# Performance work log

Measured on AMD Instinct MI355X. Metric: run time of the kernel, lower is better.

The kernel has to match this reference:

```python
import jax, jax.numpy as jnp
import numpy as np

B, T = 2, 2048
D_MODEL = 1024
N_LAYERS = 2
VOCAB = 256
BLOCK = 2048
LOCAL = 128
STRIDE = 256
NHEAD = D_MODEL // 64  # 16
HEAD_DIM = D_MODEL // NHEAD  # 64
LN_EPS = 1e-5


def setup_inputs() -> dict:
    key = jax.random.key(0)
    ks = jax.random.split(key, 16)
    L, d = N_LAYERS, D_MODEL

    def g(k, shape, scale=0.02):
        return (jax.random.normal(k, shape, dtype=jnp.float32) * scale)

    return {
        "x": jax.random.randint(ks[0], (B, T), 0, VOCAB),
        "embed": g(ks[1], (VOCAB, d)),
        "pos_embed": g(ks[2], (BLOCK, d)),
        # per-layer weights stacked on leading L axis; Linear as y = x @ W + b
        "Wq": g(ks[3], (L, d, d)), "bq": jnp.zeros((L, d), jnp.float32),
        "Wk": g(ks[4], (L, d, d)), "bk": jnp.zeros((L, d), jnp.float32),
        "Wv": g(ks[5], (L, d, d)), "bv": jnp.zeros((L, d), jnp.float32),
        "Wo": g(ks[6], (L, d, d)), "bo": jnp.zeros((L, d), jnp.float32),
        "g1": jnp.ones((L, d), jnp.float32), "be1": jnp.zeros((L, d), jnp.float32),
        "W1": g(ks[7], (L, d, 4 * d)), "bf1": jnp.zeros((L, 4 * d), jnp.float32),
        "W2": g(ks[8], (L, 4 * d, d)), "bf2": jnp.zeros((L, d), jnp.float32),
        "g2": jnp.ones((L, d), jnp.float32), "be2": jnp.zeros((L, d), jnp.float32),
        "gf": jnp.ones((d,), jnp.float32), "bef": jnp.zeros((d,), jnp.float32),
        "Whead": g(ks[9], (d, VOCAB)),
    }


def _ln(x, gamma, beta):
    mu = jnp.mean(x, axis=-1, keepdims=True)
    var = jnp.mean(jnp.square(x - mu), axis=-1, keepdims=True)
    return (x - mu) * jax.lax.rsqrt(var + LN_EPS) * gamma + beta


def _sparse_mask(t):
    # allowed[i, j] = True if token i may attend to token j
    i = jnp.arange(t)[:, None]
    j = jnp.arange(t)[None, :]
    causal = j <= i
    local = (i - j) <= LOCAL
    glob = (j % STRIDE) == 0
    return causal & (local | glob)


def _sparse_attn(q, k, v, allowed):
    # q, k, v: [B, T, D] -> [B, H, T, hd]
    b, t, d = q.shape
    def split(x):
        return x.reshape(b, t, NHEAD, HEAD_DIM).transpose(0, 2, 1, 3)
    q, k, v = split(q), split(k), split(v)
    scale = HEAD_DIM ** -0.5
    scores = jnp.einsum("bhqd,bhkd->bhqk", q, k) * scale
    scores = jnp.where(allowed[None, None], scores, -jnp.inf)
    attn = jax.nn.softmax(scores, axis=-1)  # every row has j=i allowed -> no NaN
    out = jnp.einsum("bhqk,bhkd->bhqd", attn, v)
    return out.transpose(0, 2, 1, 3).reshape(b, t, d)


def reference(x, embed, pos_embed, Wq, bq, Wk, bk, Wv, bv, Wo, bo,
              g1, be1, W1, bf1, W2, bf2, g2, be2, gf, bef, Whead):
    b, t = x.shape
    h = embed[x] + pos_embed[jnp.arange(t)][None]
    allowed = _sparse_mask(t)
    for l in range(N_LAYERS):
        h_n = _ln(h, g1[l], be1[l])
        q = h_n @ Wq[l] + bq[l]
        k = h_n @ Wk[l] + bk[l]
        v = h_n @ Wv[l] + bv[l]
        attn_out = _sparse_attn(q, k, v, allowed)
        h = h + (attn_out @ Wo[l] + bo[l])
        h2 = _ln(h, g2[l], be2[l])
        ffn = jax.nn.gelu(h2 @ W1[l] + bf1[l], approximate=False) @ W2[l] + bf2[l]
        h = h + ffn
    h = _ln(h, gf, bef)
    return h @ Whead
```

## Files before the change

kernel.cpp:

```cpp
#include <hip/hip_runtime.h>
#include <hip/hip_bf16.h>

#define BB 2
#define TT 2048
#define DD 1024
#define FF 4096
#define VV 256
#define HH 16
#define HD 64
#define MM (BB * TT)
#define LOCAL_W 128
#define STRIDE_G 256
#define QS 3072

typedef short s16x8 __attribute__((ext_vector_type(8)));
typedef __bf16 bf16x8 __attribute__((ext_vector_type(8)));
typedef float f32x4 __attribute__((ext_vector_type(4)));

#define WAITVM(N) asm volatile("s_waitcnt vmcnt(" #N ")" ::: "memory")
#define CFENCE asm volatile("" ::: "memory")

__device__ __forceinline__ float b2f(unsigned short u) {
  return __builtin_bit_cast(float, (unsigned int)u << 16);
}
__device__ __forceinline__ unsigned short f2b(float f) {
  __hip_bfloat16 h = __float2bfloat16(f);
  return __builtin_bit_cast(unsigned short, h);
}
__device__ __forceinline__ void gl_lds16(const unsigned short* g, unsigned short* l) {
  __builtin_amdgcn_global_load_lds(
      (const __attribute__((address_space(1))) void*)g,
      (__attribute__((address_space(3))) void*)l, 16, 0, 0);
}
__device__ __forceinline__ bf16x8 ldsr(const unsigned short* p) {
  return __builtin_bit_cast(bf16x8, *(const s16x8*)p);
}

__global__ __launch_bounds__(256) void transpose_k(const float* __restrict__ W,
                                                   unsigned short* __restrict__ WT,
                                                   int K, int N,
                                                   size_t sstride, size_t dstride) {
  __shared__ float t[32][33];
  const int z = blockIdx.z;
  W += (size_t)z * sstride;
  WT += (size_t)z * dstride;
  const int n0 = blockIdx.x * 32, k0 = blockIdx.y * 32;
  const int tx = threadIdx.x, ty = threadIdx.y;
  for (int r = ty; r < 32; r += 8) t[r][tx] = W[(size_t)(k0 + r) * N + n0 + tx];
  __syncthreads();
  for (int r = ty; r < 32; r += 8)
    WT[(size_t)(n0 + r) * K + k0 + tx] = f2b(t[tx][r]);
}

__global__ __launch_bounds__(256) void qkv_t(const float* __restrict__ Wq,
                                             const float* __restrict__ Wk,
                                             const float* __restrict__ Wv,
                                             unsigned short* __restrict__ WT) {
  __shared__ float t[32][33];
  const int z = blockIdx.z;
  const int l = z / 3, which = z % 3;
  const float* W = (which == 0 ? Wq : which == 1 ? Wk : Wv) + (size_t)l * DD * DD;
  unsigned short* D = WT + ((size_t)l * QS + which * DD) * DD;
  const int n0 = blockIdx.x * 32, k0 = blockIdx.y * 32;
  const int tx = threadIdx.x, ty = threadIdx.y;
  for (int r = ty; r < 32; r += 8) t[r][tx] = W[(size_t)(k0 + r) * DD + n0 + tx];
  __syncthreads();
  for (int r = ty; r < 32; r += 8)
    D[(size_t)(n0 + r) * DD + k0 + tx] = f2b(t[tx][r]);
}

__global__ __launch_bounds__(256) void concat_bias(const float* __restrict__ bq,
                                                   const float* __restrict__ bk,
                                                   const float* __restrict__ bv,
                                                   float* __restrict__ bcat) {
  const int i = blockIdx.x * 256 + threadIdx.x;
  const int l = i / QS, j = i - l * QS;
  float v;
  if (j < DD) v = bq[l * DD + j];
  else if (j < 2 * DD) v = bk[l * DD + j - DD];
  else v = bv[l * DD + j - 2 * DD];
  bcat[i] = v;
}

__global__ __launch_bounds__(256) void embed_ln(const int* __restrict__ x,
                                                const float* __restrict__ emb,
                                                const float* __restrict__ pos,
                                                const float* __restrict__ g,
                                                const float* __restrict__ be,
                                                float* __restrict__ h,
                                                unsigned short* __restrict__ out) {
  const int row = blockIdx.x;
  const int tid = threadIdx.x;
  const int tok = x[row];
  const int t = row & (TT - 1);
  f32x4 v = *(const f32x4*)&emb[(size_t)tok * DD + tid * 4];
  v += *(const f32x4*)&pos[(size_t)t * DD + tid * 4];
  *(f32x4*)&h[(size_t)row * DD + tid * 4] = v;
  float s = v[0] + v[1] + v[2] + v[3];
  float sq = v[0] * v[0] + v[1] * v[1] + v[2] * v[2] + v[3] * v[3];
#pragma unroll
  for (int off = 32; off; off >>= 1) {
    s += __shfl_xor(s, off);
    sq += __shfl_xor(sq, off);
  }
  __shared__ float ss[4], ssq[4];
  const int w = tid >> 6, lane = tid & 63;
  if (lane == 0) { ss[w] = s; ssq[w] = sq; }
  __syncthreads();
  s = ss[0] + ss[1] + ss[2] + ss[3];
  sq = ssq[0] + ssq[1] + ssq[2] + ssq[3];
  const float mean = s * (1.0f / DD);
  const float var = sq * (1.0f / DD) - mean * mean;
  const float rstd = rsqrtf(var + 1e-5f);
  const float4 gv = *(const float4*)&g[tid * 4];
  const float4 bv = *(const float4*)&be[tid * 4];
  ushort4 o;
  o.x = f2b((v[0] - mean) * rstd * gv.x + bv.x);
  o.y = f2b((v[1] - mean) * rstd * gv.y + bv.y);
  o.z = f2b((v[2] - mean) * rstd * gv.z + bv.z);
  o.w = f2b((v[3] - mean) * rstd * gv.w + bv.w);
  *(ushort4*)&out[(size_t)row * DD + tid * 4] = o;
}

__global__ __launch_bounds__(256) void ln_red(float* __restrict__ hio,
                                              const float* __restrict__ parts,
                                              const float* __restrict__ bias,
                                              const float* __restrict__ g,
                                              const float* __restrict__ be,
                                              unsigned short* __restrict__ out) {
  const int row = blockIdx.x;
  const int tid = threadIdx.x;
  const size_t base = (size_t)row * DD + tid * 4;
  f32x4 v = *(const f32x4*)&hio[base];
  v += *(const f32x4*)&bias[tid * 4];
  v += *(const f32x4*)&parts[base];
  v += *(const f32x4*)&parts[(size_t)MM * DD + base];
  *(f32x4*)&hio[base] = v;
  float s = v[0] + v[1] + v[2] + v[3];
  float sq = v[0] * v[0] + v[1] * v[1] + v[2] * v[2] + v[3] * v[3];
#pragma unroll
  for (int off = 32; off; off >>= 1) {
    s += __shfl_xor(s, off);
    sq += __shfl_xor(sq, off);
  }
  __shared__ float ss[4], ssq[4];
  const int w = tid >> 6, lane = tid & 63;
  if (lane == 0) { ss[w] = s; ssq[w] = sq; }
  __syncthreads();
  s = ss[0] + ss[1] + ss[2] + ss[3];
  sq = ssq[0] + ssq[1] + ssq[2] + ssq[3];
  const float mean = s * (1.0f / DD);
  const float var = sq * (1.0f / DD) - mean * mean;
  const float rstd = rsqrtf(var + 1e-5f);
  const float4 gv = *(const float4*)&g[tid * 4];
  const float4 bv = *(const float4*)&be[tid * 4];
  ushort4 o;
  o.x = f2b((v[0] - mean) * rstd * gv.x + bv.x);
  o.y = f2b((v[1] - mean) * rstd * gv.y + bv.y);
  o.z = f2b((v[2] - mean) * rstd * gv.z + bv.z);
  o.w = f2b((v[3] - mean) * rstd * gv.w + bv.w);
  *(ushort4*)&out[(size_t)row * DD + tid * 4] = o;
}

template <int EPI>
__global__ __launch_bounds__(512, 4) void gemm_dw3(const unsigned short* __restrict__ A,
                                                   const unsigned short* __restrict__ BT,
                                                   const float* __restrict__ bias,
                                                   void* __restrict__ outp,
                                                   int M, int N, int K,
                                                   int nbx, int nby, int ksplit,
                                                   int ksub) {
  __shared__ __align__(16) unsigned short lds[36864];
  const int tid = threadIdx.x;
  const int lane = tid & 63;
  const int w = tid >> 6;
  const int o = blockIdx.x;
  const int xcd = o & 7;
  const int j = o >> 3;
  const int m_per = (nby * ksplit) >> 2;
  const int n_per = nbx >> 1;
  const int m_loc = j % m_per, n_loc = j / m_per;
  const int m_idx = (xcd >> 1) * m_per + m_loc;
  const int n_idx = (xcd & 1) * n_per + n_loc;
  const int ks = m_idx / nby;
  const int mp = m_idx - ks * nby;
  const int n0 = n_idx * 128;
  const int m0 = mp * 256;
  const int kb = ks * ksub;
  const int wm = w >> 1, wn = w & 1;
  f32x4 acc[4][4] = {};

  const unsigned short* aSrc[2];
  const unsigned short* bSrc;
  int dstA[2], dstB;
#pragma unroll
  for (int i = 0; i < 2; i++) {
    const int s = tid + (i << 9);
    const int row = s >> 2, sc = s & 3;
    const int l = sc ^ ((row >> 1) & 3);
    aSrc[i] = &A[(size_t)(m0 + row) * K + kb + l * 8];
    dstA[i] = s * 8;
  }
  {
    const int row = tid >> 2, sc = tid & 3;
    const int l = sc ^ ((row >> 1) & 3);
    bSrc = &BT[(size_t)(n0 + row) * K + kb + l * 8];
    dstB = 8192 + tid * 8;
  }
  auto STAGE = [&](int u, int base) {
    const int kt = u << 5;
    gl_lds16(aSrc[0] + kt, &lds[base + dstA[0]]);
    gl_lds16(aSrc[1] + kt, &lds[base + dstA[1]]);
    gl_lds16(bSrc + kt, &lds[base + dstB]);
  };

  const int rA = lane & 15, cr = lane >> 4;
  const int rowA0 = wm * 64 + rA;
  const int rowB0 = wn * 64 + rA;
  const int aAddr0 = rowA0 * 32 + ((cr ^ ((rowA0 >> 1) & 3)) << 3);
  const int bAddr0 = 8192 + rowB0 * 32 + ((cr ^ ((rowB0 >> 1) & 3)) << 3);

  const int NS = ksub >> 5;
  int c0 = 0, c1 = 12288, c2 = 24576;
  STAGE(0, c0);
  STAGE(1, c1);

  for (int u = 0; u < NS; ++u) {
    if (u + 1 < NS) { WAITVM(3); } else { WAITVM(0); }
    __builtin_amdgcn_s_barrier();
    CFENCE;
    if (u + 2 < NS) STAGE(u + 2, c2);
    bf16x8 bfr[4], af[4];
#pragma unroll
    for (int n = 0; n < 4; n++) bfr[n] = ldsr(&lds[c0 + bAddr0 + n * 512]);
#pragma unroll
    for (int i = 0; i < 4; i++) af[i] = ldsr(&lds[c0 + aAddr0 + i * 512]);
    __builtin_amdgcn_s_setprio(1);
#pragma unroll
    for (int i = 0; i < 4; i++)
#pragma unroll
      for (int n = 0; n < 4; n++)
        acc[i][n] = __builtin_amdgcn_mfma_f32_16x16x32_bf16(af[i], bfr[n], acc[i][n], 0, 0, 0);
    __builtin_amdgcn_s_setprio(0);
    const int t = c0; c0 = c1; c1 = c2; c2 = t;
  }

  const int r0 = (lane >> 4) * 4;
  const int cc = lane & 15;
#pragma unroll
  for (int m = 0; m < 4; m++)
#pragma unroll
    for (int n = 0; n < 4; n++)
#pragma unroll
      for (int r = 0; r < 4; r++) {
        const int row = m0 + wm * 64 + m * 16 + r0 + r;
        const int col = n0 + wn * 64 + n * 16 + cc;
        const size_t idx = (size_t)row * N + col;
        if (EPI == 0) {
          ((float*)outp)[(size_t)ks * M * N + idx] = acc[m][n][r];
        } else {
          float val = acc[m][n][r] + bias[col];
          if (EPI == 3) {
            float u2 = val * (0.7978845608f + 0.0356774081f * val * val);
            u2 = fminf(u2, 10.0f);
            const float e = __expf(2.0f * u2);
            val = val * e / (e + 1.0f);
          }
          ((unsigned short*)outp)[idx] = f2b(val);
        }
      }
}

__global__ __launch_bounds__(512, 2) void gemm_p(const unsigned short* __restrict__ A,
                                                 const unsigned short* __restrict__ BT,
                                                 float* __restrict__ outp,
                                                 int M, int N, int K, int nbx, int nwg2,
                                                 int ksub) {
  constexpr int BM = 128;
  __shared__ __align__(16) unsigned short lds[4][BM * 64];
  const int tid = threadIdx.x;
  const int lane = tid & 63;
  const int w = tid >> 6;
  const int nwg = gridDim.x;
  const int orig = blockIdx.x;
  const int wg = (orig & 7) * (nwg >> 3) + (orig >> 3);
  const int ks = wg / nwg2;
  const int rem = wg - ks * nwg2;
  const int n0 = (rem % nbx) * BM;
  const int m0 = (rem / nbx) * BM;
  const int kb = ks * ksub;
  const int wm = w >> 2, wn = w & 3;
  f32x4 acc[4][2] = {};

  auto STAGE = [&](int t) {
    const int b = t & 3;
    const int kt = kb + (t << 5);
    const int s = tid;
    const int row = s >> 2, sc = s & 3;
    const int c = sc ^ ((row >> 1) & 3);
    gl_lds16(&A[(size_t)(m0 + row) * K + kt + c * 8], &lds[b][s * 8]);
    gl_lds16(&BT[(size_t)(n0 + row) * K + kt + c * 8], &lds[b][BM * 32 + s * 8]);
  };

  const int NT = ksub >> 5;
  STAGE(0); STAGE(1); STAGE(2);

  for (int t = 0; t < NT; ++t) {
    const int ahead = NT - 1 - t;
    if (ahead >= 2) WAITVM(4); else if (ahead == 1) WAITVM(2); else WAITVM(0);
    __builtin_amdgcn_s_barrier();
    CFENCE;
    if (t + 3 < NT) STAGE(t + 3);
    const int b = t & 3;
    const int rA = lane & 15, cr = lane >> 4;
    bf16x8 af[4], bfr[2];
#pragma unroll
    for (int m = 0; m < 4; m++) {
      const int row = wm * 64 + m * 16 + rA;
      af[m] = ldsr(&lds[b][row * 32 + ((cr ^ ((row >> 1) & 3)) << 3)]);
    }
#pragma unroll
    for (int n = 0; n < 2; n++) {
      const int row = wn * 32 + n * 16 + rA;
      bfr[n] = ldsr(&lds[b][BM * 32 + row * 32 + ((cr ^ ((row >> 1) & 3)) << 3)]);
    }
    __builtin_amdgcn_s_setprio(1);
#pragma unroll
    for (int m = 0; m < 4; m++)
#pragma unroll
      for (int n = 0; n < 2; n++)
        acc[m][n] = __builtin_amdgcn_mfma_f32_16x16x32_bf16(af[m], bfr[n], acc[m][n], 0, 0, 0);
    __builtin_amdgcn_s_setprio(0);
  }

  const int r0 = (lane >> 4) * 4;
  const int cc = lane & 15;
  float* pout = outp + (size_t)ks * M * N;
#pragma unroll
  for (int m = 0; m < 4; m++)
#pragma unroll
    for (int n = 0; n < 2; n++)
#pragma unroll
      for (int r = 0; r < 4; r++) {
        const int row = m0 + wm * 64 + m * 16 + r0 + r;
        const int col = n0 + wn * 32 + n * 16 + cc;
        pout[(size_t)row * N + col] = acc[m][n][r];
      }
}

template <int NP>
__global__ __launch_bounds__(256) void reduce_k(float* __restrict__ dst,
                                                const float* __restrict__ parts,
                                                size_t total) {
  const size_t i = ((size_t)blockIdx.x * 256 + threadIdx.x) * 4;
  if (i >= total) return;
  f32x4 acc = {};
#pragma unroll
  for (int p = 0; p < NP; p++) acc += *(const f32x4*)&parts[(size_t)p * total + i];
  *(f32x4*)&dst[i] = acc;
}

#define QT 16
#define KT 32
#define NTMAX 6
#define KP 72
#define PP 40

__global__ __launch_bounds__(256) void attn_mfma(const unsigned short* __restrict__ qkv,
                                                 unsigned short* __restrict__ outg) {
  __shared__ __align__(16) unsigned short kvs[4][KT * KP];
  __shared__ __align__(16) unsigned short pls[4][QT * PP];
  const int tid = threadIdx.x;
  const int wid = tid >> 6, lane = tid & 63;
  const int qgrp = blockIdx.x & 31;
  const int bh = blockIdx.x >> 5;
  const int h = bh & (HH - 1), b = bh >> 4;
  const size_t baseq = (size_t)b * TT * QS + (size_t)h * HD;
  const size_t baseo = (size_t)b * TT * DD + (size_t)h * HD;
  const int i0 = qgrp * 64 + wid * 16;
  const int g = lane >> 4;
  const int c = lane & 15;

  const int i0b = qgrp * 64 + 48;
  const int ka0b = (i0b > 128) ? ((i0b - 128) & ~31) : 0;
  const int nlb = ((i0b + 16 - ka0b) + 31) >> 5;
  const int neb = (ka0b + 255) >> 8;
  const int ka0 = (i0 > 128) ? ((i0 - 128) & ~31) : 0;
  const int ne = (ka0 + 255) >> 8;

  const s16x8 qf0 = *(const s16x8*)&qkv[baseq + (size_t)(i0 + c) * QS + g * 8];
  const s16x8 qf1 = *(const s16x8*)&qkv[baseq + (size_t)(i0 + c) * QS + 32 + g * 8];

  f32x4 sc[NTMAX][2];
  float smax[4] = {-1e30f, -1e30f, -1e30f, -1e30f};

#pragma unroll
  for (int t = 0; t < NTMAX; t++) {
    if (t > nlb) continue;
    const bool isg = (t == 0);
    if (isg && neb == 0) continue;
    const int kt0 = ka0 + (t - 1) * 32;
#pragma unroll
    for (int it = 0; it < 4; it++) {
      const int row = it * 8 + (lane >> 3);
      const int ch = lane & 7;
      const int j = isg ? ((row < ne) ? row * STRIDE_G : 0) : (kt0 + row);
      *(s16x8*)&kvs[wid][row * KP + ch * 8] =
          *(const s16x8*)&qkv[baseq + DD + (size_t)j * QS + ch * 8];
    }
    __syncthreads();
#pragma unroll
    for (int half = 0; half < 2; half++) {
      const int key = half * 16 + c;
      const bf16x8 kb0 = __builtin_bit_cast(bf16x8, *(const s16x8*)&kvs[wid][key * KP + g * 8]);
      const bf16x8 kb1 = __builtin_bit_cast(bf16x8, *(const s16x8*)&kvs[wid][key * KP + 32 + g * 8]);
      f32x4 a = {};
      a = __builtin_amdgcn_mfma_f32_16x16x32_bf16(__builtin_bit_cast(bf16x8, qf0), kb0, a, 0, 0, 0);
      a = __builtin_amdgcn_mfma_f32_16x16x32_bf16(__builtin_bit_cast(bf16x8, qf1), kb1, a, 0, 0, 0);
#pragma unroll
      for (int r = 0; r < 4; r++) {
        const int i = i0 + g * 4 + r;
        bool ok;
        if (isg) {
          ok = (key < ne);
        } else {
          const int j = kt0 + key;
          ok = (j <= i) && (((i - j) <= LOCAL_W) || ((j & (STRIDE_G - 1)) == 0));
        }
        const float s = ok ? a[r] * 0.125f : -1e30f;
        sc[t][half][r] = s;
        smax[r] = fmaxf(smax[r], s);
      }
    }
    __syncthreads();
  }
#pragma unroll
  for (int r = 0; r < 4; r++)
#pragma unroll
    for (int off = 8; off; off >>= 1)
      smax[r] = fmaxf(smax[r], __shfl_xor(smax[r], off));

  f32x4 o[4] = {};
  float lsum[4] = {0.f, 0.f, 0.f, 0.f};
#pragma unroll
  for (int t = 0; t < NTMAX; t++) {
    if (t > nlb) continue;
    const bool isg = (t == 0);
    if (isg && neb == 0) continue;
    const int kt0 = ka0 + (t - 1) * 32;
#pragma unroll
    for (int it = 0; it < 4; it++) {
      const int row = it * 8 + (lane >> 3);
      const int ch = lane & 7;
      const int j = isg ? ((row < ne) ? row * STRIDE_G : 0) : (kt0 + row);
      *(s16x8*)&kvs[wid][row * KP + ch * 8] =
          *(const s16x8*)&qkv[baseq + 2 * DD + (size_t)j * QS + ch * 8];
    }
#pragma unroll
    for (int half = 0; half < 2; half++)
#pragma unroll
      for (int r = 0; r < 4; r++) {
        const float p = __expf(sc[t][half][r] - smax[r]);
        lsum[r] += p;
        pls[wid][(g * 4 + r) * PP + half * 16 + c] = f2b(p);
      }
    __syncthreads();
    const bf16x8 pa = __builtin_bit_cast(bf16x8, *(const s16x8*)&pls[wid][c * PP + g * 8]);
#pragma unroll
    for (int d0 = 0; d0 < 4; d0++) {
      s16x8 bv;
#pragma unroll
      for (int e = 0; e < 8; e++)
        bv[e] = (short)kvs[wid][(g * 8 + e) * KP + d0 * 16 + c];
      o[d0] = __builtin_amdgcn_mfma_f32_16x16x32_bf16(pa, __builtin_bit_cast(bf16x8, bv), o[d0], 0, 0, 0);
    }
    __syncthreads();
  }
#pragma unroll
  for (int r = 0; r < 4; r++)
#pragma unroll
    for (int off = 8; off; off >>= 1)
      lsum[r] += __shfl_xor(lsum[r], off);
#pragma unroll
  for (int d0 = 0; d0 < 4; d0++)
#pragma unroll
    for (int r = 0; r < 4; r++)
      outg[baseo + (size_t)(i0 + g * 4 + r) * DD + d0 * 16 + c] = f2b(o[d0][r] / lsum[r]);
}

extern "C" void kernel_launch(void* const* d_in, const int* in_sizes, int n_in,
                              void* d_out, int out_size, void* d_ws, size_t ws_size,
                              hipStream_t stream) {
  const int* x = (const int*)d_in[0];
  const float* embed = (const float*)d_in[1];
  const float* pos = (const float*)d_in[2];
  const float* Wq = (const float*)d_in[3];
  const float* bq = (const float*)d_in[4];
  const float* Wk = (const float*)d_in[5];
  const float* bk = (const float*)d_in[6];
  const float* Wv = (const float*)d_in[7];
  const float* bv = (const float*)d_in[8];
  const float* Wo = (const float*)d_in[9];
  const float* bo = (const float*)d_in[10];
  const float* g1 = (const float*)d_in[11];
  const float* be1 = (const float*)d_in[12];
  const float* W1 = (const float*)d_in[13];
  const float* bf1 = (const float*)d_in[14];
  const float* W2 = (const float*)d_in[15];
  const float* bf2 = (const float*)d_in[16];
  const float* g2 = (const float*)d_in[17];
  const float* be2 = (const float*)d_in[18];
  const float* gf = (const float*)d_in[19];
  const float* bef = (const float*)d_in[20];
  const float* Whead = (const float*)d_in[21];

  char* ws = (char*)d_ws;
  size_t off = 0;
  auto alloc = [&](size_t bytes) -> void* {
    void* p = ws + off;
    off += (bytes + 255) & ~(size_t)255;
    return p;
  };
  unsigned short* WqkvT = (unsigned short*)alloc((size_t)2 * QS * DD * 2);
  unsigned short* WoT = (unsigned short*)alloc((size_t)2 * DD * DD * 2);
  unsigned short* W1T = (unsigned short*)alloc((size_t)2 * DD * FF * 2);
  unsigned short* W2T = (unsigned short*)alloc((size_t)2 * DD * FF * 2);
  unsigned short* WheadT = (unsigned short*)alloc((size_t)DD * VV * 2);
  float* bcat = (float*)alloc((size_t)2 * QS * 4);
  float* h = (float*)alloc((size_t)MM * DD * 4);
  unsigned short* hn = (unsigned short*)alloc((size_t)MM * DD * 2);
  unsigned short* qkvb = (unsigned short*)alloc((size_t)MM * QS * 2);
  unsigned short* attnb = (unsigned short*)alloc((size_t)MM * DD * 2);
  unsigned short* mid = (unsigned short*)alloc((size_t)MM * FF * 2);
  float* ffn2p = (float*)qkvb;
  float* oprojp = (float*)mid;
  float* headp = (float*)mid;
  (void)ws_size;

  const dim3 tb(32, 8);
  qkv_t<<<dim3(DD / 32, DD / 32, 6), tb, 0, stream>>>(Wq, Wk, Wv, WqkvT);
  transpose_k<<<dim3(DD / 32, DD / 32, 2), tb, 0, stream>>>(Wo, WoT, DD, DD,
                                                            (size_t)DD * DD, (size_t)DD * DD);
  transpose_k<<<dim3(FF / 32, DD / 32, 2), tb, 0, stream>>>(W1, W1T, DD, FF,
                                                            (size_t)DD * FF, (size_t)DD * FF);
  transpose_k<<<dim3(DD / 32, FF / 32, 2), tb, 0, stream>>>(W2, W2T, FF, DD,
                                                            (size_t)DD * FF, (size_t)DD * FF);
  transpose_k<<<dim3(VV / 32, DD / 32, 1), tb, 0, stream>>>(Whead, WheadT, DD, VV, 0, 0);
  concat_bias<<<24, 256, 0, stream>>>(bq, bk, bv, bcat);

  embed_ln<<<MM, 256, 0, stream>>>(x, embed, pos, g1, be1, h, hn);

  for (int l = 0; l < 2; l++) {
    const size_t wo = (size_t)l * DD * DD;
    const size_t wf = (size_t)l * DD * FF;
    gemm_dw3<1><<<(QS / 128) * (MM / 256), 512, 0, stream>>>(
        hn, WqkvT + (size_t)l * QS * DD, bcat + l * QS, qkvb,
        MM, QS, DD, QS / 128, MM / 256, 1, DD);
    attn_mfma<<<BB * HH * (TT / 64), 256, 0, stream>>>(qkvb, attnb);
    gemm_dw3<0><<<2 * (DD / 128) * (MM / 256), 512, 0, stream>>>(
        attnb, WoT + wo, nullptr, oprojp,
        MM, DD, DD, DD / 128, MM / 256, 2, DD / 2);
    ln_red<<<MM, 256, 0, stream>>>(h, oprojp, bo + l * DD, g2 + l * DD, be2 + l * DD, hn);
    gemm_dw3<3><<<(FF / 128) * (MM / 256), 512, 0, stream>>>(
        hn, W1T + wf, bf1 + l * FF, mid,
        MM, FF, DD, FF / 128, MM / 256, 1, DD);
    gemm_dw3<0><<<2 * (DD / 128) * (MM / 256), 512, 0, stream>>>(
        mid, W2T + wf, nullptr, ffn2p,
        MM, DD, FF, DD / 128, MM / 256, 2, FF / 2);
    if (l == 0)
      ln_red<<<MM, 256, 0, stream>>>(h, ffn2p, bf2, g1 + DD, be1 + DD, hn);
    else
      ln_red<<<MM, 256, 0, stream>>>(h, ffn2p, bf2 + DD, gf, bef, hn);
  }
  gemm_p<<<4 * (VV / 128) * (MM / 128), 512, 0, stream>>>(
      hn, WheadT, headp, MM, VV, DD, VV / 128, (VV / 128) * (MM / 128), DD / 4);
  reduce_k<4><<<(MM * VV) / 1024, 256, 0, stream>>>(
      (float*)d_out, headp, (size_t)MM * VV);
}
```

Measured before the change: 429.6 us.

## Replace pipelined 256x128 GEMMs with simple single-buffered 128x128 GEMM kernel

Replaces the triple-buffered 512-thread 256x128-tile GEMM and the separate head GEMM with one 256-thread 128x128-tile kernel. The new kernel loads each K-slice into a single LDS buffer and uses two __syncthreads per iteration, so loads no longer overlap with MFMA work. It cuts LDS use and register pressure and doubles the grid size, aiming for more occupancy and simpler scheduling, at the cost of losing prefetch and the setprio hints.

Result: slower. 451.1 us (+5.0%).

```diff
diff --git a/kernel.cpp b/kernel.cpp
--- a/kernel.cpp
+++ b/kernel.cpp
@@ -16,9 +16,6 @@
 typedef short s16x8 __attribute__((ext_vector_type(8)));
 typedef __bf16 bf16x8 __attribute__((ext_vector_type(8)));
 typedef float f32x4 __attribute__((ext_vector_type(4)));
-
-#define WAITVM(N) asm volatile("s_waitcnt vmcnt(" #N ")" ::: "memory")
-#define CFENCE asm volatile("" ::: "memory")
 
 __device__ __forceinline__ float b2f(unsigned short u) {
   return __builtin_bit_cast(float, (unsigned int)u << 16);
@@ -163,14 +160,14 @@
 }
 
 template <int EPI>
-__global__ __launch_bounds__(512, 4) void gemm_dw3(const unsigned short* __restrict__ A,
-                                                   const unsigned short* __restrict__ BT,
-                                                   const float* __restrict__ bias,
-                                                   void* __restrict__ outp,
-                                                   int M, int N, int K,
-                                                   int nbx, int nby, int ksplit,
-                                                   int ksub) {
-  __shared__ __align__(16) unsigned short lds[36864];
+__global__ __launch_bounds__(256, 4) void gemm_m(const unsigned short* __restrict__ A,
+                                                 const unsigned short* __restrict__ BT,
+                                                 const float* __restrict__ bias,
+                                                 void* __restrict__ outp,
+                                                 int M, int N, int K,
+                                                 int nbx, int nby, int ksplit,
+                                                 int ksub) {
+  __shared__ __align__(16) unsigned short lds[8192];
   const int tid = threadIdx.x;
   const int lane = tid & 63;
   const int w = tid >> 6;
@@ -185,64 +182,50 @@
   const int ks = m_idx / nby;
   const int mp = m_idx - ks * nby;
   const int n0 = n_idx * 128;
-  const int m0 = mp * 256;
+  const int m0 = mp * 128;
   const int kb = ks * ksub;
   const int wm = w >> 1, wn = w & 1;
   f32x4 acc[4][4] = {};
 
   const unsigned short* aSrc[2];
-  const unsigned short* bSrc;
-  int dstA[2], dstB;
+  const unsigned short* bSrc[2];
+  int dstO[2];
 #pragma unroll
   for (int i = 0; i < 2; i++) {
-    const int s = tid + (i << 9);
+    const int s = tid + (i << 8);
     const int row = s >> 2, sc = s & 3;
     const int l = sc ^ ((row >> 1) & 3);
     aSrc[i] = &A[(size_t)(m0 + row) * K + kb + l * 8];
-    dstA[i] = s * 8;
-  }
-  {
-    const int row = tid >> 2, sc = tid & 3;
-    const int l = sc ^ ((row >> 1) & 3);
-    bSrc = &BT[(size_t)(n0 + row) * K + kb + l * 8];
-    dstB = 8192 + tid * 8;
-  }
-  auto STAGE = [&](int u, int base) {
-    const int kt = u << 5;
-    gl_lds16(aSrc[0] + kt, &lds[base + dstA[0]]);
-    gl_lds16(aSrc[1] + kt, &lds[base + dstA[1]]);
-    gl_lds16(bSrc + kt, &lds[base + dstB]);
-  };
+    bSrc[i] = &BT[(size_t)(n0 + row) * K + kb + l * 8];
+    dstO[i] = s * 8;
+  }
 
   const int rA = lane & 15, cr = lane >> 4;
   const int rowA0 = wm * 64 + rA;
   const int rowB0 = wn * 64 + rA;
   const int aAddr0 = rowA0 * 32 + ((cr ^ ((rowA0 >> 1) & 3)) << 3);
-  const int bAddr0 = 8192 + rowB0 * 32 + ((cr ^ ((rowB0 >> 1) & 3)) << 3);
-
-  const int NS = ksub >> 5;
-  int c0 = 0, c1 = 12288, c2 = 24576;
-  STAGE(0, c0);
-  STAGE(1, c1);
-
-  for (int u = 0; u < NS; ++u) {
-    if (u + 1 < NS) { WAITVM(3); } else { WAITVM(0); }
-    __builtin_amdgcn_s_barrier();
-    CFENCE;
-    if (u + 2 < NS) STAGE(u + 2, c2);
-    bf16x8 bfr[4], af[4];
-#pragma unroll
-    for (int n = 0; n < 4; n++) bfr[n] = ldsr(&lds[c0 + bAddr0 + n * 512]);
-#pragma unroll
-    for (int i = 0; i < 4; i++) af[i] = ldsr(&lds[c0 + aAddr0 + i * 512]);
-    __builtin_amdgcn_s_setprio(1);
-#pragma unroll
-    for (int i = 0; i < 4; i++)
+  const int bAddr0 = 4096 + rowB0 * 32 + ((cr ^ ((rowB0 >> 1) & 3)) << 3);
+
+  const int NT = ksub >> 5;
+  for (int t = 0; t < NT; ++t) {
+    if (t) __syncthreads();
+    const int kt = t << 5;
+#pragma unroll
+    for (int i = 0; i < 2; i++) {
+      gl_lds16(aSrc[i] + kt, &lds[dstO[i]]);
+      gl_lds16(bSrc[i] + kt, &lds[4096 + dstO[i]]);
+    }
+    __syncthreads();
+    bf16x8 af[4], bfr[4];
+#pragma unroll
+    for (int m = 0; m < 4; m++) af[m] = ldsr(&lds[aAddr0 + m * 512]);
+#pragma unroll
+    for (int n = 0; n < 4; n++) bfr[n] = ldsr(&lds[bAddr0 + n * 512]);
+#pragma unroll
+    for (int m = 0; m < 4; m++)
 #pragma unroll
       for (int n = 0; n < 4; n++)
-        acc[i][n] = __builtin_amdgcn_mfma_f32_16x16x32_bf16(af[i], bfr[n], acc[i][n], 0, 0, 0);
-    __builtin_amdgcn_s_setprio(0);
-    const int t = c0; c0 = c1; c1 = c2; c2 = t;
+        acc[m][n] = __builtin_amdgcn_mfma_f32_16x16x32_bf16(af[m], bfr[n], acc[m][n], 0, 0, 0);
   }
 
   const int r0 = (lane >> 4) * 4;
@@ -268,83 +251,6 @@
           }
           ((unsigned short*)outp)[idx] = f2b(val);
         }
-      }
-}
-
-__global__ __launch_bounds__(512, 2) void gemm_p(const unsigned short* __restrict__ A,
-                                                 const unsigned short* __restrict__ BT,
-                                                 float* __restrict__ outp,
-                                                 int M, int N, int K, int nbx, int nwg2,
-                                                 int ksub) {
-  constexpr int BM = 128;
-  __shared__ __align__(16) unsigned short lds[4][BM * 64];
-  const int tid = threadIdx.x;
-  const int lane = tid & 63;
-  const int w = tid >> 6;
-  const int nwg = gridDim.x;
-  const int orig = blockIdx.x;
-  const int wg = (orig & 7) * (nwg >> 3) + (orig >> 3);
-  const int ks = wg / nwg2;
-  const int rem = wg - ks * nwg2;
-  const int n0 = (rem % nbx) * BM;
-  const int m0 = (rem / nbx) * BM;
-  const int kb = ks * ksub;
-  const int wm = w >> 2, wn = w & 3;
-  f32x4 acc[4][2] = {};
-
-  auto STAGE = [&](int t) {
-    const int b = t & 3;
-    const int kt = kb + (t << 5);
-    const int s = tid;
-    const int row = s >> 2, sc = s & 3;
-    const int c = sc ^ ((row >> 1) & 3);
-    gl_lds16(&A[(size_t)(m0 + row) * K + kt + c * 8], &lds[b][s * 8]);
-    gl_lds16(&BT[(size_t)(n0 + row) * K + kt + c * 8], &lds[b][BM * 32 + s * 8]);
-  };
-
-  const int NT = ksub >> 5;
-  STAGE(0); STAGE(1); STAGE(2);
-
-  for (int t = 0; t < NT; ++t) {
-    const int ahead = NT - 1 - t;
-    if (ahead >= 2) WAITVM(4); else if (ahead == 1) WAITVM(2); else WAITVM(0);
-    __builtin_amdgcn_s_barrier();
-    CFENCE;
-    if (t + 3 < NT) STAGE(t + 3);
-    const int b = t & 3;
-    const int rA = lane & 15, cr = lane >> 4;
-    bf16x8 af[4], bfr[2];
-#pragma unroll
-    for (int m = 0; m < 4; m++) {
-      const int row = wm * 64 + m * 16 + rA;
-      af[m] = ldsr(&lds[b][row * 32 + ((cr ^ ((row >> 1) & 3)) << 3)]);
-    }
-#pragma unroll
-    for (int n = 0; n < 2; n++) {
-      const int row = wn * 32 + n * 16 + rA;
-      bfr[n] = ldsr(&lds[b][BM * 32 + row * 32 + ((cr ^ ((row >> 1) & 3)) << 3)]);
-    }
-    __builtin_amdgcn_s_setprio(1);
-#pragma unroll
-    for (int m = 0; m < 4; m++)
-#pragma unroll
-      for (int n = 0; n < 2; n++)
-        acc[m][n] = __builtin_amdgcn_mfma_f32_16x16x32_bf16(af[m], bfr[n], acc[m][n], 0, 0, 0);
-    __builtin_amdgcn_s_setprio(0);
-  }
-
-  const int r0 = (lane >> 4) * 4;
-  const int cc = lane & 15;
-  float* pout = outp + (size_t)ks * M * N;
-#pragma unroll
-  for (int m = 0; m < 4; m++)
-#pragma unroll
-    for (int n = 0; n < 2; n++)
-#pragma unroll
-      for (int r = 0; r < 4; r++) {
-        const int row = m0 + wm * 64 + m * 16 + r0 + r;
-        const int col = n0 + wn * 32 + n * 16 + cc;
-        pout[(size_t)row * N + col] = acc[m][n][r];
       }
 }
 
@@ -553,27 +459,28 @@
   for (int l = 0; l < 2; l++) {
     const size_t wo = (size_t)l * DD * DD;
     const size_t wf = (size_t)l * DD * FF;
-    gemm_dw3<1><<<(QS / 128) * (MM / 256), 512, 0, stream>>>(
+    gemm_m<1><<<(QS / 128) * (MM / 128), 256, 0, stream>>>(
         hn, WqkvT + (size_t)l * QS * DD, bcat + l * QS, qkvb,
-        MM, QS, DD, QS / 128, MM / 256, 1, DD);
+        MM, QS, DD, QS / 128, MM / 128, 1, DD);
     attn_mfma<<<BB * HH * (TT / 64), 256, 0, stream>>>(qkvb, attnb);
-    gemm_dw3<0><<<2 * (DD / 128) * (MM / 256), 512, 0, stream>>>(
+    gemm_m<0><<<2 * (DD / 128) * (MM / 128), 256, 0, stream>>>(
         attnb, WoT + wo, nullptr, oprojp,
-        MM, DD, DD, DD / 128, MM / 256, 2, DD / 2);
+        MM, DD, DD, DD / 128, MM / 128, 2, DD / 2);
     ln_red<<<MM, 256, 0, stream>>>(h, oprojp, bo + l * DD, g2 + l * DD, be2 + l * DD, hn);
-    gemm_dw3<3><<<(FF / 128) * (MM / 256), 512, 0, stream>>>(
+    gemm_m<3><<<(FF / 128) * (MM / 128), 256, 0, stream>>>(
         hn, W1T + wf, bf1 + l * FF, mid,
-        MM, FF, DD, FF / 128, MM / 256, 1, DD);
-    gemm_dw3<0><<<2 * (DD / 128) * (MM / 256), 512, 0, stream>>>(
+        MM, FF, DD, FF / 128, MM / 128, 1, DD);
+    gemm_m<0><<<2 * (DD / 128) * (MM / 128), 256, 0, stream>>>(
         mid, W2T + wf, nullptr, ffn2p,
-        MM, DD, FF, DD / 128, MM / 256, 2, FF / 2);
+        MM, DD, FF, DD / 128, MM / 128, 2, FF / 2);
     if (l == 0)
       ln_red<<<MM, 256, 0, stream>>>(h, ffn2p, bf2, g1 + DD, be1 + DD, hn);
     else
       ln_red<<<MM, 256, 0, stream>>>(h, ffn2p, bf2 + DD, gf, bef, hn);
   }
-  gemm_p<<<4 * (VV / 128) * (MM / 128), 512, 0, stream>>>(
-      hn, WheadT, headp, MM, VV, DD, VV / 128, (VV / 128) * (MM / 128), DD / 4);
+  gemm_m<0><<<4 * (VV / 128) * (MM / 128), 256, 0, stream>>>(
+      hn, WheadT, nullptr, headp,
+      MM, VV, DD, VV / 128, MM / 128, 4, DD / 4);
   reduce_k<4><<<(MM * VV) / 1024, 256, 0, stream>>>(
       (float*)d_out, headp, (size_t)MM * VV);
 }
```
